# Performance work log

Measured on AMD Instinct MI355X. Metric: run time of the kernel, lower is better.

## Reference

```python
import jax, jax.numpy as jnp
import numpy as np

N = 100_000   # nodes
E = 1_600_000 # edges (avg degree 16)
D = 128       # in_dim == emb_dim
L = 3         # num_layer
G = 64        # num graphs in batch
EPS = 1e-5    # batchnorm eps


def setup_inputs() -> dict:
    key = jax.random.key(0)
    ks = jax.random.split(key, 8)
    x = jax.random.normal(ks[0], (N, D), dtype=jnp.float32)
    edge_index = jax.random.randint(ks[1], (2, E), 0, N)
    edge_weight = jax.random.uniform(ks[2], (E,), dtype=jnp.float32)
    batch = jnp.sort(jax.random.randint(ks[3], (N,), 0, G))
    # GCNConv linear weights (in->out) per layer, bias, and BatchNorm affine params
    W = jax.random.normal(ks[4], (L, D, D), dtype=jnp.float32) * 0.05
    b = jnp.zeros((L, D), jnp.float32)
    gamma = jnp.ones((L, D), jnp.float32)
    beta = jnp.zeros((L, D), jnp.float32)
    return dict(x=x, edge_index=edge_index, edge_weight=edge_weight,
                batch=batch, W=W, b=b, gamma=gamma, beta=beta)


def reference(x, edge_index, edge_weight, batch, W, b, gamma, beta):
    # --- GCN normalization with self loops (PyG gcn_norm, fill_value=1) ---
    loop = jnp.arange(N)
    src = jnp.concatenate([edge_index[0], loop])
    dst = jnp.concatenate([edge_index[1], loop])
    ew = jnp.concatenate([edge_weight, jnp.ones((N,), x.dtype)])
    deg = jax.ops.segment_sum(ew, dst, num_segments=N)            # [N]
    dinv = jnp.where(deg > 0, jax.lax.rsqrt(jnp.maximum(deg, 1e-12)), 0.0)
    norm = dinv[src] * ew * dinv[dst]                              # [E+N]

    for i in range(L):
        h = x @ W[i]                                               # [N, D] linear (no bias in lin)
        msg = h[src] * norm[:, None]                               # gather + scale
        out = jax.ops.segment_sum(msg, dst, num_segments=N) + b[i] # scatter-add + conv bias
        # BatchNorm1d (training-mode batch stats, biased var)
        mu = out.mean(axis=0)
        var = jnp.mean((out - mu) ** 2, axis=0)
        out = gamma[i] * (out - mu) * jax.lax.rsqrt(var + EPS) + beta[i]
        x = jax.nn.relu(out)                                       # dropout p=0 -> identity

    # sum pooling over graphs (last layer only; concat=False)
    return jax.ops.segment_sum(x, batch, num_segments=G)           # [G, D]
```

## Files before the change

### kernel.cpp

```cpp
#include <hip/hip_runtime.h>

#define NN 100000
#define NE 1600000
#define DD 128
#define NL 3
#define NG 64
#define EPSBN 1e-5f
#define NBUCK 196
#define NAGG (NN / 16)

typedef __attribute__((ext_vector_type(8))) short short8v;
typedef __attribute__((ext_vector_type(4))) float float4v;
typedef __attribute__((ext_vector_type(2))) float float2v;

__device__ inline void atomAddF(float* p, float v) {
#if defined(__AMDGCN__)
    unsafeAtomicAdd(p, v);
#else
    atomicAdd(p, v);
#endif
}

__device__ inline ushort f2bf(float f) {
    uint u = __float_as_uint(f);
    uint r = ((u >> 16) & 1u) + 0x7fffu;
    return (ushort)((u + r) >> 16);
}

__device__ inline uint f2fp8(float f) {
    return (uint)__builtin_amdgcn_cvt_pk_fp8_f32(f, f, 0, false) & 0xffu;
}

__device__ inline void accf8(float (&acc)[8], uint2 g, float wgt) {
    float2v p0 = __builtin_amdgcn_cvt_pk_f32_fp8(g.x, false);
    float2v p1 = __builtin_amdgcn_cvt_pk_f32_fp8(g.x, true);
    float2v p2 = __builtin_amdgcn_cvt_pk_f32_fp8(g.y, false);
    float2v p3 = __builtin_amdgcn_cvt_pk_f32_fp8(g.y, true);
    acc[0] = fmaf(wgt, p0[0], acc[0]);
    acc[1] = fmaf(wgt, p0[1], acc[1]);
    acc[2] = fmaf(wgt, p1[0], acc[2]);
    acc[3] = fmaf(wgt, p1[1], acc[3]);
    acc[4] = fmaf(wgt, p2[0], acc[4]);
    acc[5] = fmaf(wgt, p2[1], acc[5]);
    acc[6] = fmaf(wgt, p3[0], acc[6]);
    acc[7] = fmaf(wgt, p3[1], acc[7]);
}

__global__ __launch_bounds__(256) void k_zero_fo(const float* __restrict__ W,
                                                 ushort* __restrict__ Wt,
                                                 float* __restrict__ out,
                                                 float* __restrict__ stats,
                                                 int* __restrict__ gbcnt) {
    int i = blockIdx.x * 256 + threadIdx.x;
    if (i < NL * DD * DD) {
        int l = i >> 14, r = i & 16383;
        int k = r >> 7, n = r & 127;
        Wt[(size_t)l * DD * DD + n * DD + k] = f2bf(W[i]);
        return;
    }
    int j = i - NL * DD * DD;
    if (j < NG * DD) { out[j] = 0.f; return; }
    j -= NG * DD;
    if (j < 768) { stats[j] = 0.f; return; }
    j -= 768;
    if (j < NBUCK) gbcnt[j] = 0;
}

__global__ __launch_bounds__(256) void k_bcnt(const int* __restrict__ ei,
                                              int* __restrict__ gbcnt) {
    __shared__ int lh[NBUCK];
    int tid = threadIdx.x;
    if (tid < NBUCK) lh[tid] = 0;
    __syncthreads();
    for (int e = blockIdx.x * 256 + tid; e < NE; e += 256 * 256)
        atomicAdd(&lh[ei[NE + e] >> 9], 1);
    __syncthreads();
    if (tid < NBUCK) atomicAdd(&gbcnt[tid], lh[tid]);
}

__global__ __launch_bounds__(256) void k_bscan(const int* __restrict__ gbcnt,
                                               int* __restrict__ boff,
                                               int* __restrict__ gcur) {
    __shared__ int s[256];
    int t = threadIdx.x;
    int v = (t < NBUCK) ? gbcnt[t] : 0;
    s[t] = v;
    __syncthreads();
    for (int off = 1; off < 256; off <<= 1) {
        int add = (t >= off) ? s[t - off] : 0;
        __syncthreads();
        s[t] += add;
        __syncthreads();
    }
    if (t < NBUCK) {
        int ex = s[t] - v;
        boff[t] = ex;
        gcur[t] = ex;
    }
    if (t == NBUCK - 1) boff[NBUCK] = s[t];
}

__global__ __launch_bounds__(256) void k_bscatter(const int* __restrict__ ei,
                                                  const float* __restrict__ ew,
                                                  int* __restrict__ gcur,
                                                  int2* __restrict__ srcw) {
    __shared__ int hist[NBUCK], base[NBUCK], cur[NBUCK];
    const int tid = threadIdx.x;
    const int e0 = blockIdx.x * 6250, e1 = e0 + 6250;
    if (tid < NBUCK) hist[tid] = 0;
    __syncthreads();
    for (int e = e0 + tid; e < e1; e += 256)
        atomicAdd(&hist[ei[NE + e] >> 9], 1);
    __syncthreads();
    if (tid < NBUCK) {
        base[tid] = atomicAdd(&gcur[tid], hist[tid]);
        cur[tid] = 0;
    }
    __syncthreads();
    for (int e = e0 + tid; e < e1; e += 256) {
        int d = ei[NE + e];
        int b = d >> 9;
        int p = base[b] + atomicAdd(&cur[b], 1);
        int2 sw;
        sw.x = ei[e] | ((d & 511) << 17);
        sw.y = __float_as_int(ew[e]);
        srcw[p] = sw;
    }
}

__global__ __launch_bounds__(256) void k_bsort(const int2* __restrict__ srcw,
                                               const int* __restrict__ boff,
                                               int* __restrict__ row_off,
                                               int2* __restrict__ csr,
                                               float* __restrict__ dinv) {
    __shared__ int h0[512], h1[512], exc[512], cur[512];
    __shared__ float degacc[512];
    const int tid = threadIdx.x;
    const int b = blockIdx.x;
    const int p0 = boff[b], p1 = boff[b + 1];
    const int nbn = min(512, NN - (b << 9));

    for (int i = tid; i < 512; i += 256) {
        h0[i] = 0;
        degacc[i] = 0.f;
    }
    __syncthreads();
    for (int p = p0 + tid; p < p1; p += 256)
        atomicAdd(&h0[(srcw[p].x >> 17) & 511], 1);
    __syncthreads();

    int* sA = h0;
    int* sB = h1;
    for (int off = 1; off < 512; off <<= 1) {
        for (int i = tid; i < 512; i += 256) {
            int v = sA[i];
            if (i >= off) v += sA[i - off];
            sB[i] = v;
        }
        __syncthreads();
        int* tp = sA; sA = sB; sB = tp;
    }
    for (int i = tid; i < 512; i += 256) {
        exc[i] = (i == 0) ? 0 : sA[i - 1];
        cur[i] = 0;
    }
    __syncthreads();

    for (int n = tid; n < nbn; n += 256)
        row_off[(b << 9) + n] = p0 + exc[n];
    if (b == NBUCK - 1 && tid == 0) row_off[NN] = NE;

    for (int p = p0 + tid; p < p1; p += 256) {
        int2 sw = srcw[p];
        int dl = (sw.x >> 17) & 511;
        int q = p0 + exc[dl] + atomicAdd(&cur[dl], 1);
        int2 outv;
        outv.x = sw.x & 0x1FFFF;
        outv.y = sw.y;
        csr[q] = outv;
        atomicAdd(&degacc[dl], __int_as_float(sw.y));
    }
    __syncthreads();
    for (int n = tid; n < nbn; n += 256)
        dinv[(b << 9) + n] = rsqrtf(1.0f + degacc[n]);
}

__global__ __launch_bounds__(256, 4) void k_gemm5(const float* __restrict__ X,
                                                  const ushort* __restrict__ Xb,
                                                  const ushort* __restrict__ Wt,
                                                  const float* __restrict__ stats,
                                                  const float* __restrict__ gamma,
                                                  const float* __restrict__ beta,
                                                  int applyBN,
                                                  unsigned char* __restrict__ H) {
    __shared__ ushort ws[128 * 128];
    __shared__ float scs[DD], shs[DD];
    const int tid = threadIdx.x;

    for (int c = tid; c < 2048; c += 256) {
        int n = c >> 4, k8 = (c & 15) * 8;
        uint4 w = *(const uint4*)&Wt[n * DD + k8];
        int idx = n * 128 + (((k8 * 2) ^ ((n & 7) << 4)) >> 1);
        *(uint4*)&ws[idx] = w;
    }
    if (applyBN && tid < DD) {
        float mu = stats[tid] * (1.0f / NN);
        float var = stats[DD + tid] * (1.0f / NN) - mu * mu;
        float inv = rsqrtf(var + EPSBN);
        float s = gamma[tid] * inv;
        scs[tid] = s;
        shs[tid] = beta[tid] - mu * s;
    }
    __syncthreads();

    const int wid = tid >> 6, lane = tid & 63;
    const int lrow = lane & 15, lk = lane >> 4;
    const int gr_a = blockIdx.x * 64 + wid * 16 + lrow;

    float4v acc[8];
#pragma unroll
    for (int i = 0; i < 8; ++i) acc[i] = (float4v){0.f, 0.f, 0.f, 0.f};

#pragma unroll
    for (int ks = 0; ks < 4; ++ks) {
        const int k8 = ks * 32 + lk * 8;
        float v[8];
        if (applyBN) {
            uint4 g = (gr_a < NN) ? *(const uint4*)&Xb[(size_t)gr_a * DD + k8]
                                  : make_uint4(0u, 0u, 0u, 0u);
            v[0] = __uint_as_float(g.x << 16);
            v[1] = __uint_as_float(g.x & 0xffff0000u);
            v[2] = __uint_as_float(g.y << 16);
            v[3] = __uint_as_float(g.y & 0xffff0000u);
            v[4] = __uint_as_float(g.z << 16);
            v[5] = __uint_as_float(g.z & 0xffff0000u);
            v[6] = __uint_as_float(g.w << 16);
            v[7] = __uint_as_float(g.w & 0xffff0000u);
#pragma unroll
            for (int i = 0; i < 8; ++i)
                v[i] = fmaxf(fmaf(v[i], scs[k8 + i], shs[k8 + i]), 0.f);
        } else {
            if (gr_a < NN) {
                float4 a0 = *(const float4*)&X[(size_t)gr_a * DD + k8];
                float4 a1 = *(const float4*)&X[(size_t)gr_a * DD + k8 + 4];
                v[0] = a0.x; v[1] = a0.y; v[2] = a0.z; v[3] = a0.w;
                v[4] = a1.x; v[5] = a1.y; v[6] = a1.z; v[7] = a1.w;
            } else {
#pragma unroll
                for (int i = 0; i < 8; ++i) v[i] = 0.f;
            }
        }
        uint4 ap;
        ap.x = (uint)f2bf(v[0]) | ((uint)f2bf(v[1]) << 16);
        ap.y = (uint)f2bf(v[2]) | ((uint)f2bf(v[3]) << 16);
        ap.z = (uint)f2bf(v[4]) | ((uint)f2bf(v[5]) << 16);
        ap.w = (uint)f2bf(v[6]) | ((uint)f2bf(v[7]) << 16);
        short8v a = *(short8v*)&ap;

        const int kbyte = ks * 64 + lk * 16;
#pragma unroll
        for (int ng = 0; ng < 8; ++ng) {
            int n = ng * 16 + lrow;
            short8v b = *(const short8v*)&ws[n * 128 + ((kbyte ^ ((n & 7) << 4)) >> 1)];
            acc[ng] = __builtin_amdgcn_mfma_f32_16x16x32_bf16(a, b, acc[ng], 0, 0, 0);
        }
    }

    const int rbase = blockIdx.x * 64 + wid * 16 + lk * 4;
#pragma unroll
    for (int ng = 0; ng < 8; ++ng) {
        int col = ng * 16 + lrow;
#pragma unroll
        for (int j = 0; j < 4; ++j) {
            int gr = rbase + j;
            if (gr < NN)
                H[(size_t)gr * DD + col] = (unsigned char)f2fp8(acc[ng][j]);
        }
    }
}

__global__ __launch_bounds__(256) void k_agg3(const int2* __restrict__ csr,
                                              const int* __restrict__ row_off,
                                              const float* __restrict__ dinv,
                                              const unsigned char* __restrict__ H,
                                              ushort* __restrict__ Ab,
                                              float* __restrict__ partial) {
    __shared__ float sbv[16][128];
    __shared__ float sbq[16][128];
    const int tid = threadIdx.x;
    int node = blockIdx.x * 16 + (tid >> 4);
    int h = tid & 15;
    int beg = row_off[node], end = row_off[node + 1];
    float dv = dinv[node];
    size_t cb = (size_t)node * DD + h * 8;
    float acc[8] = {0.f, 0.f, 0.f, 0.f, 0.f, 0.f, 0.f, 0.f};
    {
        uint2 v = *(const uint2*)&H[cb];
        accf8(acc, v, dv);
    }

    int j = beg;
    for (; j + 8 <= end; j += 8) {
        int2 e0 = csr[j], e1 = csr[j + 1], e2 = csr[j + 2], e3 = csr[j + 3];
        int2 e4 = csr[j + 4], e5 = csr[j + 5], e6 = csr[j + 6], e7 = csr[j + 7];
        float w0 = __int_as_float(e0.y) * dinv[e0.x];
        float w1 = __int_as_float(e1.y) * dinv[e1.x];
        float w2 = __int_as_float(e2.y) * dinv[e2.x];
        float w3 = __int_as_float(e3.y) * dinv[e3.x];
        float w4 = __int_as_float(e4.y) * dinv[e4.x];
        float w5 = __int_as_float(e5.y) * dinv[e5.x];
        float w6 = __int_as_float(e6.y) * dinv[e6.x];
        float w7 = __int_as_float(e7.y) * dinv[e7.x];
        uint2 g0 = *(const uint2*)&H[(size_t)e0.x * DD + h * 8];
        uint2 g1 = *(const uint2*)&H[(size_t)e1.x * DD + h * 8];
        uint2 g2 = *(const uint2*)&H[(size_t)e2.x * DD + h * 8];
        uint2 g3 = *(const uint2*)&H[(size_t)e3.x * DD + h * 8];
        uint2 g4 = *(const uint2*)&H[(size_t)e4.x * DD + h * 8];
        uint2 g5 = *(const uint2*)&H[(size_t)e5.x * DD + h * 8];
        uint2 g6 = *(const uint2*)&H[(size_t)e6.x * DD + h * 8];
        uint2 g7 = *(const uint2*)&H[(size_t)e7.x * DD + h * 8];
        accf8(acc, g0, w0);
        accf8(acc, g1, w1);
        accf8(acc, g2, w2);
        accf8(acc, g3, w3);
        accf8(acc, g4, w4);
        accf8(acc, g5, w5);
        accf8(acc, g6, w6);
        accf8(acc, g7, w7);
    }
    for (; j + 4 <= end; j += 4) {
        int2 e0 = csr[j], e1 = csr[j + 1], e2 = csr[j + 2], e3 = csr[j + 3];
        float w0 = __int_as_float(e0.y) * dinv[e0.x];
        float w1 = __int_as_float(e1.y) * dinv[e1.x];
        float w2 = __int_as_float(e2.y) * dinv[e2.x];
        float w3 = __int_as_float(e3.y) * dinv[e3.x];
        uint2 g0 = *(const uint2*)&H[(size_t)e0.x * DD + h * 8];
        uint2 g1 = *(const uint2*)&H[(size_t)e1.x * DD + h * 8];
        uint2 g2 = *(const uint2*)&H[(size_t)e2.x * DD + h * 8];
        uint2 g3 = *(const uint2*)&H[(size_t)e3.x * DD + h * 8];
        accf8(acc, g0, w0);
        accf8(acc, g1, w1);
        accf8(acc, g2, w2);
        accf8(acc, g3, w3);
    }
    for (; j < end; ++j) {
        int2 e = csr[j];
        float w = __int_as_float(e.y) * dinv[e.x];
        uint2 g = *(const uint2*)&H[(size_t)e.x * DD + h * 8];
        accf8(acc, g, w);
    }

#pragma unroll
    for (int i = 0; i < 8; ++i) acc[i] *= dv;

    uint4 st;
    st.x = (uint)f2bf(acc[0]) | ((uint)f2bf(acc[1]) << 16);
    st.y = (uint)f2bf(acc[2]) | ((uint)f2bf(acc[3]) << 16);
    st.z = (uint)f2bf(acc[4]) | ((uint)f2bf(acc[5]) << 16);
    st.w = (uint)f2bf(acc[6]) | ((uint)f2bf(acc[7]) << 16);
    *(uint4*)&Ab[cb] = st;

    int n = tid >> 4, c0 = h * 8;
#pragma unroll
    for (int i = 0; i < 8; ++i) {
        float a = acc[i];
        sbv[n][c0 + i] = a;
        sbq[n][c0 + i] = a * a;
    }
    __syncthreads();
    float s = 0.f;
    if (tid < 128) {
#pragma unroll
        for (int k = 0; k < 16; ++k) s += sbv[k][tid];
    } else {
        int c = tid - 128;
#pragma unroll
        for (int k = 0; k < 16; ++k) s += sbq[k][c];
    }
    partial[(size_t)blockIdx.x * 256 + tid] = s;
}

__global__ __launch_bounds__(256) void k_bn_red(const float* __restrict__ partial,
                                                float* __restrict__ stats) {
    int r0 = blockIdx.x * 25;
    int r1 = min(r0 + 25, NAGG);
    int t = threadIdx.x;
    float s = 0.f;
    for (int r = r0; r < r1; ++r) s += partial[(size_t)r * 256 + t];
    atomAddF(&stats[t], s);
}

__global__ __launch_bounds__(256) void k_pool(const ushort* __restrict__ Ab,
                                              const int* __restrict__ batch,
                                              const float* __restrict__ stats,
                                              const float* __restrict__ gamma,
                                              const float* __restrict__ beta,
                                              float* __restrict__ out) {
    __shared__ int bsh[512];
    __shared__ float scs[DD], shs[DD];
    const int tid = threadIdx.x;
    const int lane = tid & 15, rg = tid >> 4;
    const int c0 = lane * 8;
    const int v0 = blockIdx.x * 512;
    const int v1 = min(v0 + 512, NN);
    for (int i = tid; i < v1 - v0; i += 256) bsh[i] = batch[v0 + i];
    if (tid < DD) {
        float mu = stats[tid] * (1.0f / NN);
        float var = stats[DD + tid] * (1.0f / NN) - mu * mu;
        float inv = rsqrtf(var + EPSBN);
        float s = gamma[tid] * inv;
        scs[tid] = s;
        shs[tid] = beta[tid] - mu * s;
    }
    __syncthreads();

    float s[8], t[8];
#pragma unroll
    for (int i = 0; i < 8; ++i) {
        s[i] = scs[c0 + i];
        t[i] = shs[c0 + i];
    }
    float acc[8] = {0.f, 0.f, 0.f, 0.f, 0.f, 0.f, 0.f, 0.f};
    int g = -1;
    for (int v = v0 + rg; v < v1; v += 16) {
        int bg = bsh[v - v0];
        if (bg != g) {
            if (g >= 0) {
                float* op = &out[(size_t)g * DD + c0];
#pragma unroll
                for (int i = 0; i < 8; ++i) atomAddF(op + i, acc[i]);
            }
            g = bg;
#pragma unroll
            for (int i = 0; i < 8; ++i) acc[i] = 0.f;
        }
        uint4 a = *(const uint4*)&Ab[(size_t)v * DD + c0];
        float x0 = __uint_as_float(a.x << 16);
        float x1 = __uint_as_float(a.x & 0xffff0000u);
        float x2 = __uint_as_float(a.y << 16);
        float x3 = __uint_as_float(a.y & 0xffff0000u);
        float x4 = __uint_as_float(a.z << 16);
        float x5 = __uint_as_float(a.z & 0xffff0000u);
        float x6 = __uint_as_float(a.w << 16);
        float x7 = __uint_as_float(a.w & 0xffff0000u);
        acc[0] += fmaxf(fmaf(x0, s[0], t[0]), 0.f);
        acc[1] += fmaxf(fmaf(x1, s[1], t[1]), 0.f);
        acc[2] += fmaxf(fmaf(x2, s[2], t[2]), 0.f);
        acc[3] += fmaxf(fmaf(x3, s[3], t[3]), 0.f);
        acc[4] += fmaxf(fmaf(x4, s[4], t[4]), 0.f);
        acc[5] += fmaxf(fmaf(x5, s[5], t[5]), 0.f);
        acc[6] += fmaxf(fmaf(x6, s[6], t[6]), 0.f);
        acc[7] += fmaxf(fmaf(x7, s[7], t[7]), 0.f);
    }
    if (g >= 0) {
        float* op = &out[(size_t)g * DD + c0];
#pragma unroll
        for (int i = 0; i < 8; ++i) atomAddF(op + i, acc[i]);
    }
}

extern "C" void kernel_launch(void* const* d_in, const int* in_sizes, int n_in,
                              void* d_out, int out_size, void* d_ws, size_t ws_size,
                              hipStream_t stream) {
    const float* x     = (const float*)d_in[0];
    const int*   ei    = (const int*)d_in[1];
    const float* ew    = (const float*)d_in[2];
    const int*   batch = (const int*)d_in[3];
    const float* W     = (const float*)d_in[4];
    const float* gamma = (const float*)d_in[6];
    const float* beta  = (const float*)d_in[7];
    float* out = (float*)d_out;

    float* wsp   = (float*)d_ws;
    float* dinv  = wsp;
    float* stats = dinv + NN;
    ushort* Wt   = (ushort*)(stats + 768);
    unsigned char* H = (unsigned char*)(Wt + (size_t)NL * DD * DD);
    ushort* Ab   = (ushort*)(H + (size_t)NN * DD);
    int2*  srcw  = (int2*)(Ab + (size_t)NN * DD);
    float* partial = (float*)(srcw + NE);
    int*   row_off = (int*)(partial + (size_t)NAGG * 256);
    int*   gbcnt = row_off + NN + 4;
    int*   boff  = gbcnt + NBUCK;
    int*   gcur  = boff + NBUCK + 4;
    int2*  csr   = (int2*)(gcur + NBUCK);

    k_zero_fo<<<(NL * DD * DD + NG * DD + 768 + NBUCK + 255) / 256, 256, 0,
                stream>>>(W, Wt, out, stats, gbcnt);

    k_bcnt<<<256, 256, 0, stream>>>(ei, gbcnt);
    k_bscan<<<1, 256, 0, stream>>>(gbcnt, boff, gcur);
    k_bscatter<<<256, 256, 0, stream>>>(ei, ew, gcur, srcw);
    k_bsort<<<NBUCK, 256, 0, stream>>>(srcw, boff, row_off, csr, dinv);

    for (int l = 0; l < NL; ++l) {
        const float* st_prev = stats + (l - 1) * 256;
        const float* ga_prev = gamma + (size_t)(l > 0 ? l - 1 : 0) * DD;
        const float* be_prev = beta + (size_t)(l > 0 ? l - 1 : 0) * DD;
        k_gemm5<<<(NN + 63) / 64, 256, 0, stream>>>(
            x, Ab, Wt + (size_t)l * DD * DD, l > 0 ? st_prev : stats,
            ga_prev, be_prev, l > 0 ? 1 : 0, H);
        k_agg3<<<NAGG, 256, 0, stream>>>(csr, row_off, dinv, H, Ab, partial);
        k_bn_red<<<(NAGG + 24) / 25, 256, 0, stream>>>(partial, stats + l * 256);
    }

    k_pool<<<NBUCK, 256, 0, stream>>>(Ab, batch, stats + 2 * 256,
                                      gamma + 2 * DD, beta + 2 * DD, out);
}
```

Measured before the change: 316.0 us.

## Use per-block bucket histograms to drop the recount pass and zero kernel

Weight transposition and zeroing of the output and BN stats are folded into the bucket-count kernel, removing one launch. Each count block now handles the same edge range its scatter block later uses and writes a per-block histogram. The single-block scan turns these into per-block prefixes plus bucket offsets. The scatter kernel then needs neither its own histogram pass over the destination indices nor global atomics for its base offsets. The cost is a single-block scan that walks 256 block histograms serially, plus extra workspace for the histogram and prefix arrays.

```diff
diff --git a/kernel.cpp b/kernel.cpp
--- a/kernel.cpp
+++ b/kernel.cpp
@@ -8,6 +8,7 @@
 #define EPSBN 1e-5f
 #define NBUCK 196
 #define NAGG (NN / 16)
+#define NSCAT 256
 
 typedef __attribute__((ext_vector_type(8))) short short8v;
 typedef __attribute__((ext_vector_type(4))) float float4v;
@@ -46,77 +47,74 @@
     acc[7] = fmaf(wgt, p3[1], acc[7]);
 }
 
-__global__ __launch_bounds__(256) void k_zero_fo(const float* __restrict__ W,
-                                                 ushort* __restrict__ Wt,
-                                                 float* __restrict__ out,
-                                                 float* __restrict__ stats,
-                                                 int* __restrict__ gbcnt) {
-    int i = blockIdx.x * 256 + threadIdx.x;
-    if (i < NL * DD * DD) {
-        int l = i >> 14, r = i & 16383;
+__global__ __launch_bounds__(256) void k_bcnt2(const int* __restrict__ ei,
+                                               const float* __restrict__ W,
+                                               ushort* __restrict__ Wt,
+                                               float* __restrict__ out,
+                                               float* __restrict__ stats,
+                                               int* __restrict__ hist) {
+    __shared__ int lh[NBUCK];
+    const int tid = threadIdx.x;
+    if (tid < NBUCK) lh[tid] = 0;
+    __syncthreads();
+
+    int gi = blockIdx.x * 256 + tid;
+    if (gi < NL * DD * DD) {
+        int l = gi >> 14, r = gi & 16383;
         int k = r >> 7, n = r & 127;
-        Wt[(size_t)l * DD * DD + n * DD + k] = f2bf(W[i]);
-        return;
-    }
-    int j = i - NL * DD * DD;
-    if (j < NG * DD) { out[j] = 0.f; return; }
-    j -= NG * DD;
-    if (j < 768) { stats[j] = 0.f; return; }
-    j -= 768;
-    if (j < NBUCK) gbcnt[j] = 0;
-}
-
-__global__ __launch_bounds__(256) void k_bcnt(const int* __restrict__ ei,
-                                              int* __restrict__ gbcnt) {
-    __shared__ int lh[NBUCK];
-    int tid = threadIdx.x;
-    if (tid < NBUCK) lh[tid] = 0;
-    __syncthreads();
-    for (int e = blockIdx.x * 256 + tid; e < NE; e += 256 * 256)
+        Wt[(size_t)l * DD * DD + n * DD + k] = f2bf(W[gi]);
+    } else {
+        int j = gi - NL * DD * DD;
+        if (j < NG * DD) out[j] = 0.f;
+        else if (j - NG * DD < 768) stats[j - NG * DD] = 0.f;
+    }
+
+    const int e0 = blockIdx.x * 6250, e1 = e0 + 6250;
+    for (int e = e0 + tid; e < e1; e += 256)
         atomicAdd(&lh[ei[NE + e] >> 9], 1);
     __syncthreads();
-    if (tid < NBUCK) atomicAdd(&gbcnt[tid], lh[tid]);
-}
-
-__global__ __launch_bounds__(256) void k_bscan(const int* __restrict__ gbcnt,
-                                               int* __restrict__ boff,
-                                               int* __restrict__ gcur) {
+    if (tid < NBUCK) hist[blockIdx.x * NBUCK + tid] = lh[tid];
+}
+
+__global__ __launch_bounds__(256) void k_bscan2(const int* __restrict__ hist,
+                                                int* __restrict__ prefix,
+                                                int* __restrict__ boff) {
     __shared__ int s[256];
     int t = threadIdx.x;
-    int v = (t < NBUCK) ? gbcnt[t] : 0;
-    s[t] = v;
-    __syncthreads();
+    int cum = 0;
+    if (t < NBUCK) {
+        for (int blk = 0; blk < NSCAT; ++blk) {
+            int v = hist[blk * NBUCK + t];
+            prefix[blk * NBUCK + t] = cum;
+            cum += v;
+        }
+    }
+    s[t] = (t < NBUCK) ? cum : 0;
+    __syncthreads();
+    int v = s[t];
     for (int off = 1; off < 256; off <<= 1) {
         int add = (t >= off) ? s[t - off] : 0;
         __syncthreads();
         s[t] += add;
         __syncthreads();
     }
-    if (t < NBUCK) {
-        int ex = s[t] - v;
-        boff[t] = ex;
-        gcur[t] = ex;
-    }
+    if (t < NBUCK) boff[t] = s[t] - v;
     if (t == NBUCK - 1) boff[NBUCK] = s[t];
 }
 
-__global__ __launch_bounds__(256) void k_bscatter(const int* __restrict__ ei,
-                                                  const float* __restrict__ ew,
-                                                  int* __restrict__ gcur,
-                                                  int2* __restrict__ srcw) {
-    __shared__ int hist[NBUCK], base[NBUCK], cur[NBUCK];
+__global__ __launch_bounds__(256) void k_bscatter2(const int* __restrict__ ei,
+                                                   const float* __restrict__ ew,
+                                                   const int* __restrict__ prefix,
+                                                   const int* __restrict__ boff,
+                                                   int2* __restrict__ srcw) {
+    __shared__ int base[NBUCK], cur[NBUCK];
     const int tid = threadIdx.x;
+    if (tid < NBUCK) {
+        base[tid] = boff[tid] + prefix[blockIdx.x * NBUCK + tid];
+        cur[tid] = 0;
+    }
+    __syncthreads();
     const int e0 = blockIdx.x * 6250, e1 = e0 + 6250;
-    if (tid < NBUCK) hist[tid] = 0;
-    __syncthreads();
-    for (int e = e0 + tid; e < e1; e += 256)
-        atomicAdd(&hist[ei[NE + e] >> 9], 1);
-    __syncthreads();
-    if (tid < NBUCK) {
-        base[tid] = atomicAdd(&gcur[tid], hist[tid]);
-        cur[tid] = 0;
-    }
-    __syncthreads();
     for (int e = e0 + tid; e < e1; e += 256) {
         int d = ei[NE + e];
         int b = d >> 9;
@@ -480,17 +478,14 @@
     int2*  srcw  = (int2*)(Ab + (size_t)NN * DD);
     float* partial = (float*)(srcw + NE);
     int*   row_off = (int*)(partial + (size_t)NAGG * 256);
-    int*   gbcnt = row_off + NN + 4;
-    int*   boff  = gbcnt + NBUCK;
-    int*   gcur  = boff + NBUCK + 4;
-    int2*  csr   = (int2*)(gcur + NBUCK);
-
-    k_zero_fo<<<(NL * DD * DD + NG * DD + 768 + NBUCK + 255) / 256, 256, 0,
-                stream>>>(W, Wt, out, stats, gbcnt);
-
-    k_bcnt<<<256, 256, 0, stream>>>(ei, gbcnt);
-    k_bscan<<<1, 256, 0, stream>>>(gbcnt, boff, gcur);
-    k_bscatter<<<256, 256, 0, stream>>>(ei, ew, gcur, srcw);
+    int*   hist  = row_off + NN + 4;
+    int*   prefix = hist + NSCAT * NBUCK;
+    int*   boff  = prefix + NSCAT * NBUCK;
+    int2*  csr   = (int2*)(boff + NBUCK + 4);
+
+    k_bcnt2<<<NSCAT, 256, 0, stream>>>(ei, W, Wt, out, stats, hist);
+    k_bscan2<<<1, 256, 0, stream>>>(hist, prefix, boff);
+    k_bscatter2<<<NSCAT, 256, 0, stream>>>(ei, ew, prefix, boff, srcw);
     k_bsort<<<NBUCK, 256, 0, stream>>>(srcw, boff, row_off, csr, dinv);
 
     for (int l = 0; l < NL; ++l) {
```

Measured after the change: 312.2 us. Within noise of the previous version (-1.2%).
